# Kernel tuning notes

Measured on AMD Instinct MI355X. Metric: run time of the kernel, lower is better.

The kernel has to match this reference:

```python
import jax, jax.numpy as jnp
import numpy as np

N, E = 50000, 800000
C_IN, C_OUT, HID = 64, 64, 64


def setup_inputs() -> dict:
    key = jax.random.key(0)
    ks = jax.random.split(key, 12)
    def rn(k, shape, scale=0.05):
        return jax.random.normal(k, shape, dtype=jnp.float32) * scale
    return dict(
        x=jax.random.normal(ks[0], (N, C_IN), dtype=jnp.float32),
        pos=jax.random.normal(ks[1], (N, 3), dtype=jnp.float32),
        edge_index=jax.random.randint(ks[2], (2, E), 0, N),
        W_in=rn(ks[3], (C_IN, C_IN)), b_in=jnp.zeros((C_IN,), jnp.float32),
        W_out=rn(ks[4], (C_OUT, C_OUT)), b_out=jnp.zeros((C_OUT,), jnp.float32),
        W_lin=rn(ks[5], (C_OUT, C_IN)),   # PointTransformerConv.lin (value), bias=False
        W_src=rn(ks[6], (C_OUT, C_IN)),   # lin_src, bias=False
        W_dst=rn(ks[7], (C_OUT, C_IN)),   # lin_dst, bias=False
        pos_w1=rn(ks[8], (HID, 3)), pos_b1=jnp.zeros((HID,), jnp.float32),
        pos_w2=rn(ks[9], (C_OUT, HID)), pos_b2=jnp.zeros((C_OUT,), jnp.float32),
        att_w1=rn(ks[10], (HID, C_OUT)), att_b1=jnp.zeros((HID,), jnp.float32),
        att_w2=rn(ks[11], (C_OUT, HID)), att_b2=jnp.zeros((C_OUT,), jnp.float32),
    )


def _mlp2(y, w1, b1, w2, b2):
    # MLP([a, 64, b], batch_norm=False): Linear->ReLU->Linear->ReLU
    y = jax.nn.relu(y @ w1.T + b1)
    return jax.nn.relu(y @ w2.T + b2)


def reference(x, pos, edge_index, W_in, b_in, W_out, b_out, W_lin, W_src, W_dst,
              pos_w1, pos_b1, pos_w2, pos_b2, att_w1, att_b1, att_w2, att_b2):
    n = x.shape[0]
    h = jax.nn.relu(x @ W_in.T + b_in)            # lin_in + relu, (N, C_in)
    v = h @ W_lin.T                                # value projection (N, C_out)
    k_src = h @ W_src.T                            # alpha_j source part
    q_dst = h @ W_dst.T                            # alpha_i dest part
    # PointTransformerConv adds self-loops by default
    loop = jnp.arange(n)
    src = jnp.concatenate([edge_index[0], loop])   # (E+N,)
    dst = jnp.concatenate([edge_index[1], loop])
    # per-edge positional encoding: pos_nn(pos_i - pos_j)
    delta = _mlp2(pos[dst] - pos[src], pos_w1, pos_b1, pos_w2, pos_b2)
    # per-edge attention logits: attn_nn(alpha_i - alpha_j), (E+N, C_out)
    alpha = _mlp2(q_dst[dst] - k_src[src], att_w1, att_b1, att_w2, att_b2)
    # per-destination-node channelwise softmax (self-loops ensure no empty segment)
    amax = jax.ops.segment_max(alpha, dst, num_segments=n)
    ex = jnp.exp(alpha - amax[dst])
    denom = jax.ops.segment_sum(ex, dst, num_segments=n)
    w = ex / (denom[dst] + 1e-16)
    # message = alpha * (x_j + delta); aggregate = sum over neighbors
    out = jax.ops.segment_sum(w * (v[src] + delta), dst, num_segments=n)
    return jax.nn.relu(out @ W_out.T + b_out)
```

## Files before the change

### kernel.cpp

```cpp
#include <hip/hip_runtime.h>
#include <math.h>

#define NN 50000
#define EE 800000
#define ET (EE + NN)
#define C  64
#define NBLK 49
#define NCHUNK 831
#define ZBLK 463

typedef __attribute__((ext_vector_type(8))) _Float16 f16x8;
typedef __attribute__((ext_vector_type(4))) _Float16 f16x4;
typedef __attribute__((ext_vector_type(2))) _Float16 f16x2;
typedef __attribute__((ext_vector_type(4))) float f32x4;

__device__ __forceinline__ f16x2 pk2(float a, float b) {
  return __builtin_bit_cast(f16x2, __builtin_amdgcn_cvt_pkrtz(a, b));
}
__device__ __forceinline__ f16x4 pk4(float a, float b, float c, float d) {
  return __builtin_shufflevector(pk2(a, b), pk2(c, d), 0, 1, 2, 3);
}
__device__ __forceinline__ f16x8 pk8(const float* y) {
  const f16x4 lo = pk4(y[0], y[1], y[2], y[3]);
  const f16x4 hi = pk4(y[4], y[5], y[6], y[7]);
  return __builtin_shufflevector(lo, hi, 0, 1, 2, 3, 4, 5, 6, 7);
}

__device__ __forceinline__ f16x8 frag_ldh(const _Float16* base, int row,
                                          int kofs) {
  return *(const f16x8*)(base + row * 72 + kofs);
}
__device__ __forceinline__ void stage_w(_Float16* __restrict__ dst,
                                        const _Float16* __restrict__ src16,
                                        int tid) {
  const f16x8* src = (const f16x8*)(src16 + tid * 16);
  _Float16* d = dst + (tid >> 2) * 72 + (tid & 3) * 16;
  ((f16x8*)d)[0] = src[0];
  ((f16x8*)d)[1] = src[1];
}

__device__ __forceinline__ int swzb(int row, int colbyte) {
  return row * 128 + (colbyte ^ ((row & 7) << 4));
}
__device__ __forceinline__ f16x8 frag_lds(const _Float16* base, int row,
                                          int kofs) {
  return *(const f16x8*)((const char*)base + swzb(row, kofs * 2));
}
__device__ __forceinline__ void stage_ws(_Float16* __restrict__ dst,
                                         const _Float16* __restrict__ src16,
                                         int tid) {
  const f16x8* src = (const f16x8*)(src16 + tid * 16);
  const int row = tid >> 2;
  const int c0 = (tid & 3) * 32;
  *(f16x8*)((char*)dst + swzb(row, c0)) = src[0];
  *(f16x8*)((char*)dst + swzb(row, c0 + 16)) = src[1];
}

__device__ __forceinline__ int psl(int e, int o) {
  return (e + 2 * o + (o >> 5)) & 63;
}

__global__ __launch_bounds__(256) void prep_kernel(
    const float* __restrict__ W_in, const float* __restrict__ W_lin,
    const float* __restrict__ W_src, const float* __restrict__ W_dst,
    const float* __restrict__ att_w1, const float* __restrict__ att_w2,
    const float* __restrict__ pos_w2, const float* __restrict__ W_out,
    _Float16* __restrict__ w16, int* __restrict__ cnt2) {
  if (blockIdx.x < 8) {
    const float* Ws[8] = {W_in, W_lin, W_src, W_dst, att_w1, att_w2, pos_w2,
                          W_out};
    const float* src = Ws[blockIdx.x];
    _Float16* dst = w16 + blockIdx.x * 4096;
    const float sc = (blockIdx.x == 5) ? 1.44269504088896340736f : 1.0f;
#pragma unroll
    for (int i = threadIdx.x * 4; i < 4096; i += 1024) {
      const float4 w = *(const float4*)(src + i);
      *(f16x4*)(dst + i) = pk4(w.x * sc, w.y * sc, w.z * sc, w.w * sc);
    }
  }
  int4* cz = (int4*)cnt2;
#pragma unroll 1
  for (int i = blockIdx.x * 256 + threadIdx.x; i < 2 * NN; i += 64 * 256)
    cz[i] = make_int4(0, 0, 0, 0);
}

__global__ __launch_bounds__(256) void scan_partial(const int* __restrict__ cnt2,
                                                    int* __restrict__ bsum,
                                                    float* __restrict__ zeroreg) {
  const int t = threadIdx.x;
  if (blockIdx.x >= NBLK) {
    const int zb = blockIdx.x - NBLK;
    float4* dst = (float4*)zeroreg;
    const int total4 = 2 * NN * 64 / 4;
    const float4 z = make_float4(0.f, 0.f, 0.f, 0.f);
#pragma unroll 1
    for (int i = zb * 256 + t; i < total4; i += ZBLK * 256) dst[i] = z;
    return;
  }
  __shared__ int ws[4];
  const int base = blockIdx.x * 1024 + t * 4;
  int s = 0;
  if (base + 3 < NN) {
#pragma unroll
    for (int sh = 0; sh < 8; ++sh) {
      const int4 v = *(const int4*)(cnt2 + sh * NN + base);
      s += v.x + v.y + v.z + v.w;
    }
  } else {
#pragma unroll
    for (int i = 0; i < 4; ++i)
      if (base + i < NN)
#pragma unroll
        for (int sh = 0; sh < 8; ++sh) s += cnt2[sh * NN + base + i];
  }
#pragma unroll
  for (int off = 32; off; off >>= 1) s += __shfl_down(s, off, 64);
  if ((t & 63) == 0) ws[t >> 6] = s;
  __syncthreads();
  if (t == 0) bsum[blockIdx.x] = ws[0] + ws[1] + ws[2] + ws[3];
}

__global__ __launch_bounds__(256) void scan_final(const int* __restrict__ cnt2,
                                                  const int* __restrict__ bsum,
                                                  int* __restrict__ curs2) {
  __shared__ int tsum[256];
  __shared__ int sblk[64];
  const int t = threadIdx.x;
  if (t < 64) {
    const int mine = (t < NBLK) ? bsum[t] : 0;
    int v = mine;
#pragma unroll
    for (int off = 1; off < 64; off <<= 1) {
      const int u = __shfl_up(v, off, 64);
      if (t >= off) v += u;
    }
    sblk[t] = v - mine;
  }
  const int base = blockIdx.x * 1024 + t * 4;
  int c2[8][4];
  int v[4] = {0, 0, 0, 0};
  if (base + 3 < NN) {
#pragma unroll
    for (int sh = 0; sh < 8; ++sh) {
      const int4 x = *(const int4*)(cnt2 + sh * NN + base);
      c2[sh][0] = x.x; c2[sh][1] = x.y; c2[sh][2] = x.z; c2[sh][3] = x.w;
      v[0] += x.x; v[1] += x.y; v[2] += x.z; v[3] += x.w;
    }
  } else {
#pragma unroll
    for (int sh = 0; sh < 8; ++sh)
#pragma unroll
      for (int i = 0; i < 4; ++i) {
        const int c = (base + i < NN) ? cnt2[sh * NN + base + i] : 0;
        c2[sh][i] = c;
        v[i] += c;
      }
  }
  const int s = v[0] + v[1] + v[2] + v[3];
  tsum[t] = s;
  __syncthreads();
  for (int off = 1; off < 256; off <<= 1) {
    const int u = (t >= off) ? tsum[t - off] : 0;
    __syncthreads();
    tsum[t] += u;
    __syncthreads();
  }
  int ex = sblk[blockIdx.x] + tsum[t] - s;
  int offs[8][4];
#pragma unroll
  for (int i = 0; i < 4; ++i) {
    int run = ex;
#pragma unroll
    for (int sh = 0; sh < 8; ++sh) {
      offs[sh][i] = run;
      run += c2[sh][i];
    }
    ex += v[i];
  }
  if (base + 3 < NN) {
#pragma unroll
    for (int sh = 0; sh < 8; ++sh)
      *(int4*)(curs2 + sh * NN + base) =
          make_int4(offs[sh][0], offs[sh][1], offs[sh][2], offs[sh][3]);
  } else {
#pragma unroll
    for (int sh = 0; sh < 8; ++sh)
#pragma unroll
      for (int i = 0; i < 4; ++i)
        if (base + i < NN) curs2[sh * NN + base + i] = offs[sh][i];
  }
}

__global__ __launch_bounds__(256) void scatter_kernel(const int* __restrict__ ei,
                                                      int* __restrict__ curs2,
                                                      int2* __restrict__ srt) {
  const int chunk = blockIdx.x;
  int* cs = curs2 + (chunk & 7) * NN;
  const int e0 = chunk * 1024 + threadIdx.x * 4;
  if (e0 >= ET) return;
  int s[4], d[4];
  if (e0 + 3 < EE) {
    const int4 sv = *(const int4*)(ei + e0);
    const int4 dv = *(const int4*)(ei + EE + e0);
    s[0] = sv.x; s[1] = sv.y; s[2] = sv.z; s[3] = sv.w;
    d[0] = dv.x; d[1] = dv.y; d[2] = dv.z; d[3] = dv.w;
  } else {
#pragma unroll
    for (int i = 0; i < 4; ++i) {
      const int e = e0 + i;
      if (e < EE) {
        s[i] = ei[e];
        d[i] = ei[EE + e];
      } else if (e < ET) {
        s[i] = d[i] = e - EE;
      } else {
        s[i] = d[i] = -1;
      }
    }
  }
#pragma unroll
  for (int i = 0; i < 4; ++i) {
    if (d[i] >= 0) {
      const int p = atomicAdd(&cs[d[i]], 1);
      srt[p] = make_int2(s[i], d[i]);
    }
  }
}

__global__ __launch_bounds__(256, 3) void node_proj(
    const float* __restrict__ x, const float* __restrict__ b_in,
    const _Float16* __restrict__ w16, const int* __restrict__ ei,
    int* __restrict__ cnt2, _Float16* __restrict__ vh,
    _Float16* __restrict__ kh, _Float16* __restrict__ qh) {
  __shared__ __align__(16) _Float16 wlds[4 * 4608];
  __shared__ __align__(16) _Float16 hlds[4608];
  __shared__ float biasv[64];

  const int tid = threadIdx.x;
  const int nb = blockIdx.x * 64;
  const int l15 = tid & 15;
  const int quad = (tid >> 4) & 3;
  const int wband = tid >> 6;
  const int nloc = wband * 16 + l15;
  const int gn = nb + nloc;

#pragma unroll 1
  for (int chunk = blockIdx.x; chunk < NCHUNK; chunk += gridDim.x) {
    int* cs = cnt2 + (chunk & 7) * NN;
    const int e0 = chunk * 1024 + tid * 4;
    if (e0 < ET) {
      int d[4];
      if (e0 + 3 < EE) {
        const int4 dv = *(const int4*)(ei + EE + e0);
        d[0] = dv.x; d[1] = dv.y; d[2] = dv.z; d[3] = dv.w;
      } else {
#pragma unroll
        for (int i = 0; i < 4; ++i) {
          const int e = e0 + i;
          d[i] = (e < EE) ? ei[EE + e] : ((e < ET) ? e - EE : -1);
        }
      }
#pragma unroll
      for (int i = 0; i < 4; ++i)
        if (d[i] >= 0) atomicAdd(&cs[d[i]], 1);
    }
  }

#pragma unroll
  for (int w = 0; w < 4; ++w) stage_w(wlds + w * 4608, w16 + w * 4096, tid);
  if (tid < 64) biasv[tid] = b_in[tid];

  f16x8 bfrag[2];
#pragma unroll
  for (int ks = 0; ks < 2; ++ks) {
    float y[8] = {0.f, 0.f, 0.f, 0.f, 0.f, 0.f, 0.f, 0.f};
    if (gn < NN) {
      const float4 a = *(const float4*)(x + (size_t)gn * 64 + ks * 32 + quad * 8);
      const float4 b = *(const float4*)(x + (size_t)gn * 64 + ks * 32 + quad * 8 + 4);
      y[0] = a.x; y[1] = a.y; y[2] = a.z; y[3] = a.w;
      y[4] = b.x; y[5] = b.y; y[6] = b.z; y[7] = b.w;
    }
    bfrag[ks] = pk8(y);
  }
  __syncthreads();

#pragma unroll
  for (int t = 0; t < 4; ++t) {
    f32x4 acc = {0.f, 0.f, 0.f, 0.f};
#pragma unroll
    for (int ks = 0; ks < 2; ++ks) {
      const f16x8 af = frag_ldh(wlds, t * 16 + l15, ks * 32 + quad * 8);
      acc = __builtin_amdgcn_mfma_f32_16x16x32_f16(af, bfrag[ks], acc, 0, 0, 0);
    }
    const int hb = t * 16 + quad * 4;
    *(f16x4*)(hlds + nloc * 72 + hb) =
        pk4(fmaxf(acc[0] + biasv[hb + 0], 0.f), fmaxf(acc[1] + biasv[hb + 1], 0.f),
            fmaxf(acc[2] + biasv[hb + 2], 0.f), fmaxf(acc[3] + biasv[hb + 3], 0.f));
  }
  __syncthreads();

  f16x8 hfrag[2];
#pragma unroll
  for (int ks = 0; ks < 2; ++ks)
    hfrag[ks] = frag_ldh(hlds, nloc, ks * 32 + quad * 8);

  _Float16* outs[3] = {vh, kh, qh};
#pragma unroll
  for (int p = 0; p < 3; ++p) {
    const _Float16* W = wlds + (p + 1) * 4608;
#pragma unroll
    for (int t = 0; t < 4; ++t) {
      f32x4 acc = {0.f, 0.f, 0.f, 0.f};
#pragma unroll
      for (int ks = 0; ks < 2; ++ks) {
        const f16x8 af = frag_ldh(W, t * 16 + l15, ks * 32 + quad * 8);
        acc = __builtin_amdgcn_mfma_f32_16x16x32_f16(af, hfrag[ks], acc, 0, 0, 0);
      }
      if (gn < NN) {
        *(f16x4*)(outs[p] + (size_t)gn * 64 + t * 16 + quad * 4) =
            pk4(acc[0], acc[1], acc[2], acc[3]);
      }
    }
  }
}

__global__ __launch_bounds__(256, 6) void edge_pass(
    const int2* __restrict__ srt, const float* __restrict__ pos,
    const _Float16* __restrict__ vh, const _Float16* __restrict__ kh,
    const _Float16* __restrict__ qh, const _Float16* __restrict__ w16,
    const float* __restrict__ att_b1, const float* __restrict__ att_b2,
    const float* __restrict__ pos_w1, const float* __restrict__ pos_b1,
    const float* __restrict__ pos_b2, float* __restrict__ num,
    float* __restrict__ den) {
  __shared__ __align__(16) _Float16 smem[12288];
  __shared__ __align__(16) float posw1T[3 * 64];
  __shared__ float b1s[64], b2s[64], pb1s[64], pb2s[64];
  __shared__ int dsts[64];

  _Float16* W1 = smem;
  _Float16* W2 = smem + 4096;
  _Float16* HP = smem + 8192;
  f16x2* pairb = (f16x2*)smem;

  const int tid = threadIdx.x;
  const int eb = blockIdx.x * 64;
  const int l15 = tid & 15;
  const int quad = (tid >> 4) & 3;
  const int wband = tid >> 6;
  const int eloc = wband * 16 + l15;

  int s_mine, d_mine;
  f16x8 bfrag[2];
  float dp0, dp1, dp2;
  {
    const int e = eb + eloc;
    int2 sd = make_int2(0, 0);
    int valid_d = -1;
    if (e < ET) {
      sd = srt[e];
      valid_d = sd.y;
    }
    s_mine = sd.x;
    d_mine = sd.y;
    if (quad == 0) dsts[eloc] = valid_d;
#pragma unroll
    for (int ks = 0; ks < 2; ++ks) {
      const f16x8 qv =
          *(const f16x8*)(qh + (size_t)d_mine * 64 + ks * 32 + quad * 8);
      const f16x8 kv =
          *(const f16x8*)(kh + (size_t)s_mine * 64 + ks * 32 + quad * 8);
      bfrag[ks] = qv - kv;
    }
    dp0 = pos[(size_t)d_mine * 3 + 0] - pos[(size_t)s_mine * 3 + 0];
    dp1 = pos[(size_t)d_mine * 3 + 1] - pos[(size_t)s_mine * 3 + 1];
    dp2 = pos[(size_t)d_mine * 3 + 2] - pos[(size_t)s_mine * 3 + 2];
  }

  stage_ws(W1, w16 + 4 * 4096, tid);
  stage_ws(W2, w16 + 5 * 4096, tid);
  if (tid < 64) {
    b1s[tid] = att_b1[tid];
    b2s[tid] = att_b2[tid] * 1.44269504088896340736f;
    pb1s[tid] = pos_b1[tid];
    pb2s[tid] = pos_b2[tid];
    posw1T[0 * 64 + tid] = pos_w1[tid * 3 + 0];
    posw1T[1 * 64 + tid] = pos_w1[tid * 3 + 1];
    posw1T[2 * 64 + tid] = pos_w1[tid * 3 + 2];
  }
  __syncthreads();

#pragma unroll
  for (int t = 0; t < 4; ++t) {
    f32x4 acc = {0.f, 0.f, 0.f, 0.f};
#pragma unroll
    for (int ks = 0; ks < 2; ++ks) {
      const f16x8 af = frag_lds(W1, t * 16 + l15, ks * 32 + quad * 8);
      acc = __builtin_amdgcn_mfma_f32_16x16x32_f16(af, bfrag[ks], acc, 0, 0, 0);
    }
    const int hb = t * 16 + quad * 4;
    *(f16x4*)((char*)HP + swzb(eloc, hb * 2)) =
        pk4(fmaxf(acc[0] + b1s[hb + 0], 0.f), fmaxf(acc[1] + b1s[hb + 1], 0.f),
            fmaxf(acc[2] + b1s[hb + 2], 0.f), fmaxf(acc[3] + b1s[hb + 3], 0.f));
  }

  f16x8 hpfrag[2];
#pragma unroll
  for (int ks = 0; ks < 2; ++ks) {
    float hv[8];
#pragma unroll
    for (int j = 0; j < 8; ++j) {
      const int i = ks * 32 + quad * 8 + j;
      float h = pb1s[i];
      h = fmaf(dp0, posw1T[i], h);
      h = fmaf(dp1, posw1T[64 + i], h);
      h = fmaf(dp2, posw1T[128 + i], h);
      hv[j] = fmaxf(h, 0.f);
    }
    hpfrag[ks] = pk8(hv);
  }

  float ex[16];
  {
    f16x8 hfrag[2];
#pragma unroll
    for (int ks = 0; ks < 2; ++ks)
      hfrag[ks] = frag_lds(HP, eloc, ks * 32 + quad * 8);
#pragma unroll
    for (int t = 0; t < 4; ++t) {
      f32x4 acc = {0.f, 0.f, 0.f, 0.f};
#pragma unroll
      for (int ks = 0; ks < 2; ++ks) {
        const f16x8 af = frag_lds(W2, t * 16 + l15, ks * 32 + quad * 8);
        acc = __builtin_amdgcn_mfma_f32_16x16x32_f16(af, hfrag[ks], acc, 0, 0, 0);
      }
      const int ob = t * 16 + quad * 4;
#pragma unroll
      for (int r = 0; r < 4; ++r)
        ex[t * 4 + r] = __builtin_exp2f(fmaxf(acc[r] + b2s[ob + r], 0.f));
    }
  }
  float vr[16];
#pragma unroll
  for (int t = 0; t < 4; ++t) {
    const f16x4 v4 = *(const f16x4*)(vh + (size_t)s_mine * 64 + t * 16 + quad * 4);
    vr[t * 4 + 0] = (float)v4[0];
    vr[t * 4 + 1] = (float)v4[1];
    vr[t * 4 + 2] = (float)v4[2];
    vr[t * 4 + 3] = (float)v4[3];
  }
  __syncthreads();

  stage_ws(HP, w16 + 6 * 4096, tid);
  __syncthreads();

  float del[16];
#pragma unroll
  for (int t = 0; t < 4; ++t) {
    f32x4 acc = {0.f, 0.f, 0.f, 0.f};
#pragma unroll
    for (int ks = 0; ks < 2; ++ks) {
      const f16x8 af = frag_lds(HP, t * 16 + l15, ks * 32 + quad * 8);
      acc = __builtin_amdgcn_mfma_f32_16x16x32_f16(af, hpfrag[ks], acc, 0, 0, 0);
    }
    const int ob = t * 16 + quad * 4;
#pragma unroll
    for (int r = 0; r < 4; ++r)
      del[t * 4 + r] = fmaxf(acc[r] + pb2s[ob + r], 0.f);
  }

#pragma unroll
  for (int t = 0; t < 4; ++t) {
#pragma unroll
    for (int r = 0; r < 4; ++r) {
      const int o = t * 16 + quad * 4 + r;
      const float e_ = ex[t * 4 + r];
      pairb[o * 64 + psl(eloc, o)] =
          pk2(e_ * (vr[t * 4 + r] + del[t * 4 + r]), e_);
    }
  }
  __syncthreads();

  {
    const int c = tid & 63;
    const int r = tid >> 6;
    float am = 0.f, ae = 0.f;
    int cur = -1;
#pragma unroll 1
    for (int t2 = 0; t2 < 16; ++t2) {
      const int el = r * 16 + t2;
      const int d = dsts[el];
      if (d != cur) {
        if (cur >= 0) {
          unsafeAtomicAdd(num + (size_t)cur * 64 + c, am);
          unsafeAtomicAdd(den + (size_t)cur * 64 + c, ae);
        }
        cur = d;
        am = 0.f;
        ae = 0.f;
      }
      if (d >= 0) {
        const f16x2 pe = pairb[c * 64 + psl(el, c)];
        am += (float)pe[0];
        ae += (float)pe[1];
      }
    }
    if (cur >= 0) {
      unsafeAtomicAdd(num + (size_t)cur * 64 + c, am);
      unsafeAtomicAdd(den + (size_t)cur * 64 + c, ae);
    }
  }
}

__global__ __launch_bounds__(256, 4) void out_proj(
    const float* __restrict__ num, const float* __restrict__ den,
    const _Float16* __restrict__ w16, const float* __restrict__ b_out,
    float* __restrict__ out) {
  __shared__ __align__(16) _Float16 wlds[4608];
  __shared__ float biasv[64];

  const int tid = threadIdx.x;
  const int nb = blockIdx.x * 64;
  const int l15 = tid & 15;
  const int quad = (tid >> 4) & 3;
  const int wband = tid >> 6;
  const int gn = nb + wband * 16 + l15;

  stage_w(wlds, w16 + 7 * 4096, tid);
  if (tid < 64) biasv[tid] = b_out[tid];

  f16x8 bfrag[2];
#pragma unroll
  for (int ks = 0; ks < 2; ++ks) {
    float y[8] = {0.f, 0.f, 0.f, 0.f, 0.f, 0.f, 0.f, 0.f};
    if (gn < NN) {
      const size_t base = (size_t)gn * 64 + ks * 32 + quad * 8;
      const float4 n0 = *(const float4*)(num + base);
      const float4 n1 = *(const float4*)(num + base + 4);
      const float4 d0 = *(const float4*)(den + base);
      const float4 d1 = *(const float4*)(den + base + 4);
      y[0] = n0.x / (d0.x + 1e-16f); y[1] = n0.y / (d0.y + 1e-16f);
      y[2] = n0.z / (d0.z + 1e-16f); y[3] = n0.w / (d0.w + 1e-16f);
      y[4] = n1.x / (d1.x + 1e-16f); y[5] = n1.y / (d1.y + 1e-16f);
      y[6] = n1.z / (d1.z + 1e-16f); y[7] = n1.w / (d1.w + 1e-16f);
    }
    bfrag[ks] = pk8(y);
  }
  __syncthreads();

#pragma unroll
  for (int t = 0; t < 4; ++t) {
    f32x4 acc = {0.f, 0.f, 0.f, 0.f};
#pragma unroll
    for (int ks = 0; ks < 2; ++ks) {
      const f16x8 af = frag_ldh(wlds, t * 16 + l15, ks * 32 + quad * 8);
      acc = __builtin_amdgcn_mfma_f32_16x16x32_f16(af, bfrag[ks], acc, 0, 0, 0);
    }
    if (gn < NN) {
      const int ob = t * 16 + quad * 4;
      float4 r;
      r.x = fmaxf(acc[0] + biasv[ob + 0], 0.f);
      r.y = fmaxf(acc[1] + biasv[ob + 1], 0.f);
      r.z = fmaxf(acc[2] + biasv[ob + 2], 0.f);
      r.w = fmaxf(acc[3] + biasv[ob + 3], 0.f);
      *(float4*)(out + (size_t)gn * 64 + ob) = r;
    }
  }
}

extern "C" void kernel_launch(void* const* d_in, const int* in_sizes, int n_in,
                              void* d_out, int out_size, void* d_ws,
                              size_t ws_size, hipStream_t stream) {
  const float* x      = (const float*)d_in[0];
  const float* pos    = (const float*)d_in[1];
  const int*   ei     = (const int*)d_in[2];
  const float* W_in   = (const float*)d_in[3];
  const float* b_in   = (const float*)d_in[4];
  const float* W_out  = (const float*)d_in[5];
  const float* b_out  = (const float*)d_in[6];
  const float* W_lin  = (const float*)d_in[7];
  const float* W_src  = (const float*)d_in[8];
  const float* W_dst  = (const float*)d_in[9];
  const float* pos_w1 = (const float*)d_in[10];
  const float* pos_b1 = (const float*)d_in[11];
  const float* pos_w2 = (const float*)d_in[12];
  const float* pos_b2 = (const float*)d_in[13];
  const float* att_w1 = (const float*)d_in[14];
  const float* att_b1 = (const float*)d_in[15];
  const float* att_w2 = (const float*)d_in[16];
  const float* att_b2 = (const float*)d_in[17];

  float* ws = (float*)d_ws;
  const size_t NC = (size_t)NN * C;
  float* num = ws;
  float* den = ws + NC;
  _Float16* vh = (_Float16*)(ws + 2 * NC);
  _Float16* kh = vh + NC;
  _Float16* qh = kh + NC;
  _Float16* w16 = qh + NC;
  int* ib     = (int*)(w16 + 8 * 4096);
  int* cnt2   = ib;
  int* curs2  = ib + 8 * NN;
  int* bsum   = ib + 16 * NN;
  int2* srt   = (int2*)(((uintptr_t)(bsum + NBLK) + 15) & ~(uintptr_t)15);

  const dim3 blk(256);
  prep_kernel<<<dim3(64), blk, 0, stream>>>(W_in, W_lin, W_src, W_dst, att_w1,
                                            att_w2, pos_w2, W_out, w16, cnt2);
  node_proj<<<dim3((NN + 63) / 64), blk, 0, stream>>>(x, b_in, w16, ei, cnt2,
                                                      vh, kh, qh);
  scan_partial<<<dim3(NBLK + ZBLK), blk, 0, stream>>>(cnt2, bsum, num);
  scan_final<<<dim3(NBLK), blk, 0, stream>>>(cnt2, bsum, curs2);
  scatter_kernel<<<dim3(NCHUNK), blk, 0, stream>>>(ei, curs2, srt);
  edge_pass<<<dim3((ET + 63) / 64), blk, 0, stream>>>(
      srt, pos, vh, kh, qh, w16, att_b1, att_b2, pos_w1, pos_b1, pos_b2, num,
      den);
  out_proj<<<dim3((NN + 63) / 64), blk, 0, stream>>>(num, den, w16, b_out,
                                                     (float*)d_out);
}
```

Measured before the change: 291.5 us.

## Double edge_pass block to 128 edges with 512 threads and reuse shared memory

The edge pass now processes 128 edges per block with 512 threads instead of 64 edges with 256 threads. Staging of the attention and positional-MLP weights is therefore spread over twice as many edges. The positional weight matrix now reuses the first attention weight buffer, and an extra barrier was added because the enlarged pair buffer overlaps it. Launch bounds change to 512 threads with a higher occupancy hint, which may raise register pressure and cause spills. The extra barrier and larger per-block shared memory footprint could also reduce overlap between blocks.

```diff
diff --git a/kernel.cpp b/kernel.cpp
--- a/kernel.cpp
+++ b/kernel.cpp
@@ -8,6 +8,8 @@
 #define NBLK 49
 #define NCHUNK 831
 #define ZBLK 463
+#define EB 128
+#define NEBLK ((ET + EB - 1) / EB)
 
 typedef __attribute__((ext_vector_type(8))) _Float16 f16x8;
 typedef __attribute__((ext_vector_type(4))) _Float16 f16x4;
@@ -46,18 +48,15 @@
                                           int kofs) {
   return *(const f16x8*)((const char*)base + swzb(row, kofs * 2));
 }
-__device__ __forceinline__ void stage_ws(_Float16* __restrict__ dst,
-                                         const _Float16* __restrict__ src16,
-                                         int tid) {
-  const f16x8* src = (const f16x8*)(src16 + tid * 16);
-  const int row = tid >> 2;
-  const int c0 = (tid & 3) * 32;
-  *(f16x8*)((char*)dst + swzb(row, c0)) = src[0];
-  *(f16x8*)((char*)dst + swzb(row, c0 + 16)) = src[1];
+__device__ __forceinline__ void stage_ws512(_Float16* __restrict__ dst,
+                                            const _Float16* __restrict__ src16,
+                                            int tid) {
+  const f16x8 v = *(const f16x8*)(src16 + tid * 8);
+  *(f16x8*)((char*)dst + swzb(tid >> 3, (tid & 7) * 16)) = v;
 }
 
 __device__ __forceinline__ int psl(int e, int o) {
-  return (e + 2 * o + (o >> 5)) & 63;
+  return (e + 2 * o + (o >> 5)) & 127;
 }
 
 __global__ __launch_bounds__(256) void prep_kernel(
@@ -324,7 +323,7 @@
   }
 }
 
-__global__ __launch_bounds__(256, 6) void edge_pass(
+__global__ __launch_bounds__(512, 8) void edge_pass(
     const int2* __restrict__ srt, const float* __restrict__ pos,
     const _Float16* __restrict__ vh, const _Float16* __restrict__ kh,
     const _Float16* __restrict__ qh, const _Float16* __restrict__ w16,
@@ -332,10 +331,10 @@
     const float* __restrict__ pos_w1, const float* __restrict__ pos_b1,
     const float* __restrict__ pos_b2, float* __restrict__ num,
     float* __restrict__ den) {
-  __shared__ __align__(16) _Float16 smem[12288];
+  __shared__ __align__(16) _Float16 smem[16384];
   __shared__ __align__(16) float posw1T[3 * 64];
   __shared__ float b1s[64], b2s[64], pb1s[64], pb2s[64];
-  __shared__ int dsts[64];
+  __shared__ int dsts[EB];
 
   _Float16* W1 = smem;
   _Float16* W2 = smem + 4096;
@@ -343,7 +342,7 @@
   f16x2* pairb = (f16x2*)smem;
 
   const int tid = threadIdx.x;
-  const int eb = blockIdx.x * 64;
+  const int eb = blockIdx.x * EB;
   const int l15 = tid & 15;
   const int quad = (tid >> 4) & 3;
   const int wband = tid >> 6;
@@ -376,8 +375,8 @@
     dp2 = pos[(size_t)d_mine * 3 + 2] - pos[(size_t)s_mine * 3 + 2];
   }
 
-  stage_ws(W1, w16 + 4 * 4096, tid);
-  stage_ws(W2, w16 + 5 * 4096, tid);
+  stage_ws512(W1, w16 + 4 * 4096, tid);
+  stage_ws512(W2, w16 + 5 * 4096, tid);
   if (tid < 64) {
     b1s[tid] = att_b1[tid];
     b2s[tid] = att_b2[tid] * 1.44269504088896340736f;
@@ -450,7 +449,7 @@
   }
   __syncthreads();
 
-  stage_ws(HP, w16 + 6 * 4096, tid);
+  stage_ws512(W1, w16 + 6 * 4096, tid);
   __syncthreads();
 
   float del[16];
@@ -459,7 +458,7 @@
     f32x4 acc = {0.f, 0.f, 0.f, 0.f};
 #pragma unroll
     for (int ks = 0; ks < 2; ++ks) {
-      const f16x8 af = frag_lds(HP, t * 16 + l15, ks * 32 + quad * 8);
+      const f16x8 af = frag_lds(W1, t * 16 + l15, ks * 32 + quad * 8);
       acc = __builtin_amdgcn_mfma_f32_16x16x32_f16(af, hpfrag[ks], acc, 0, 0, 0);
     }
     const int ob = t * 16 + quad * 4;
@@ -467,6 +466,7 @@
     for (int r = 0; r < 4; ++r)
       del[t * 4 + r] = fmaxf(acc[r] + pb2s[ob + r], 0.f);
   }
+  __syncthreads();
 
 #pragma unroll
   for (int t = 0; t < 4; ++t) {
@@ -474,7 +474,7 @@
     for (int r = 0; r < 4; ++r) {
       const int o = t * 16 + quad * 4 + r;
       const float e_ = ex[t * 4 + r];
-      pairb[o * 64 + psl(eloc, o)] =
+      pairb[o * EB + psl(eloc, o)] =
           pk2(e_ * (vr[t * 4 + r] + del[t * 4 + r]), e_);
     }
   }
@@ -499,7 +499,7 @@
         ae = 0.f;
       }
       if (d >= 0) {
-        const f16x2 pe = pairb[c * 64 + psl(el, c)];
+        const f16x2 pe = pairb[c * EB + psl(el, c)];
         am += (float)pe[0];
         ae += (float)pe[1];
       }
@@ -611,7 +611,7 @@
   scan_partial<<<dim3(NBLK + ZBLK), blk, 0, stream>>>(cnt2, bsum, num);
   scan_final<<<dim3(NBLK), blk, 0, stream>>>(cnt2, bsum, curs2);
   scatter_kernel<<<dim3(NCHUNK), blk, 0, stream>>>(ei, curs2, srt);
-  edge_pass<<<dim3((ET + 63) / 64), blk, 0, stream>>>(
+  edge_pass<<<dim3(NEBLK), dim3(512), 0, stream>>>(
       srt, pos, vh, kh, qh, w16, att_b1, att_b2, pos_w1, pos_b1, pos_b2, num,
       den);
   out_proj<<<dim3((NN + 63) / 64), blk, 0, stream>>>(num, den, w16, b_out,
```

Measured after the change: 305.1 us. +4.7%, slower.

## Swap MFMA operands so edge results land per-channel and scatter from registers

Applied to the files above, without the earlier changes.

The second attention MLP layer and the positional MLP layer now pass activations as the A operand and weights as B. Each lane therefore holds four consecutive edges for one channel, and the segmented reduction and atomics run straight from registers. This removes the shared-memory pair buffer transpose and one barrier, and the value rows are gathered per channel up front. The cost is shorter run merging: only four edges per lane instead of sixteen per thread, which may mean more atomic operations, and the per-element 2-byte value gathers are less coalesced.

```diff
diff --git a/kernel.cpp b/kernel.cpp
--- a/kernel.cpp
+++ b/kernel.cpp
@@ -54,10 +54,6 @@
   const int c0 = (tid & 3) * 32;
   *(f16x8*)((char*)dst + swzb(row, c0)) = src[0];
   *(f16x8*)((char*)dst + swzb(row, c0 + 16)) = src[1];
-}
-
-__device__ __forceinline__ int psl(int e, int o) {
-  return (e + 2 * o + (o >> 5)) & 63;
 }
 
 __global__ __launch_bounds__(256) void prep_kernel(
@@ -336,11 +332,11 @@
   __shared__ __align__(16) float posw1T[3 * 64];
   __shared__ float b1s[64], b2s[64], pb1s[64], pb2s[64];
   __shared__ int dsts[64];
+  __shared__ int srcs[64];
 
   _Float16* W1 = smem;
   _Float16* W2 = smem + 4096;
   _Float16* HP = smem + 8192;
-  f16x2* pairb = (f16x2*)smem;
 
   const int tid = threadIdx.x;
   const int eb = blockIdx.x * 64;
@@ -362,7 +358,10 @@
     }
     s_mine = sd.x;
     d_mine = sd.y;
-    if (quad == 0) dsts[eloc] = valid_d;
+    if (quad == 0) {
+      dsts[eloc] = valid_d;
+      srcs[eloc] = sd.x;
+    }
 #pragma unroll
     for (int ks = 0; ks < 2; ++ks) {
       const f16x8 qv =
@@ -389,6 +388,27 @@
   }
   __syncthreads();
 
+  int d4[4], s4[4];
+#pragma unroll
+  for (int r = 0; r < 4; ++r) {
+    d4[r] = dsts[wband * 16 + quad * 4 + r];
+    s4[r] = srcs[wband * 16 + quad * 4 + r];
+  }
+  _Float16 vvh[16];
+#pragma unroll
+  for (int r = 0; r < 4; ++r) {
+    const int sr = (d4[r] >= 0) ? s4[r] : 0;
+    const _Float16* vp = vh + (size_t)sr * 64 + l15;
+#pragma unroll
+    for (int tc = 0; tc < 4; ++tc) vvh[tc * 4 + r] = vp[tc * 16];
+  }
+  float b2v[4], pb2v[4];
+#pragma unroll
+  for (int tc = 0; tc < 4; ++tc) {
+    b2v[tc] = b2s[tc * 16 + l15];
+    pb2v[tc] = pb2s[tc * 16 + l15];
+  }
+
 #pragma unroll
   for (int t = 0; t < 4; ++t) {
     f32x4 acc = {0.f, 0.f, 0.f, 0.f};
@@ -419,94 +439,67 @@
     hpfrag[ks] = pk8(hv);
   }
 
-  float ex[16];
+  float exq[16];
   {
     f16x8 hfrag[2];
 #pragma unroll
     for (int ks = 0; ks < 2; ++ks)
       hfrag[ks] = frag_lds(HP, eloc, ks * 32 + quad * 8);
 #pragma unroll
-    for (int t = 0; t < 4; ++t) {
+    for (int tc = 0; tc < 4; ++tc) {
       f32x4 acc = {0.f, 0.f, 0.f, 0.f};
 #pragma unroll
       for (int ks = 0; ks < 2; ++ks) {
-        const f16x8 af = frag_lds(W2, t * 16 + l15, ks * 32 + quad * 8);
-        acc = __builtin_amdgcn_mfma_f32_16x16x32_f16(af, hfrag[ks], acc, 0, 0, 0);
-      }
-      const int ob = t * 16 + quad * 4;
+        const f16x8 bw = frag_lds(W2, tc * 16 + l15, ks * 32 + quad * 8);
+        acc = __builtin_amdgcn_mfma_f32_16x16x32_f16(hfrag[ks], bw, acc, 0, 0, 0);
+      }
 #pragma unroll
       for (int r = 0; r < 4; ++r)
-        ex[t * 4 + r] = __builtin_exp2f(fmaxf(acc[r] + b2s[ob + r], 0.f));
-    }
-  }
-  float vr[16];
-#pragma unroll
-  for (int t = 0; t < 4; ++t) {
-    const f16x4 v4 = *(const f16x4*)(vh + (size_t)s_mine * 64 + t * 16 + quad * 4);
-    vr[t * 4 + 0] = (float)v4[0];
-    vr[t * 4 + 1] = (float)v4[1];
-    vr[t * 4 + 2] = (float)v4[2];
-    vr[t * 4 + 3] = (float)v4[3];
-  }
-  __syncthreads();
-
-  stage_ws(HP, w16 + 6 * 4096, tid);
-  __syncthreads();
-
-  float del[16];
-#pragma unroll
-  for (int t = 0; t < 4; ++t) {
+        exq[tc * 4 + r] = __builtin_exp2f(fmaxf(acc[r] + b2v[tc], 0.f));
+    }
+  }
+  __syncthreads();
+
+  stage_ws(W1, w16 + 6 * 4096, tid);
+  __syncthreads();
+
+#pragma unroll
+  for (int tc = 0; tc < 4; ++tc) {
     f32x4 acc = {0.f, 0.f, 0.f, 0.f};
 #pragma unroll
     for (int ks = 0; ks < 2; ++ks) {
-      const f16x8 af = frag_lds(HP, t * 16 + l15, ks * 32 + quad * 8);
-      acc = __builtin_amdgcn_mfma_f32_16x16x32_f16(af, hpfrag[ks], acc, 0, 0, 0);
-    }
-    const int ob = t * 16 + quad * 4;
-#pragma unroll
-    for (int r = 0; r < 4; ++r)
-      del[t * 4 + r] = fmaxf(acc[r] + pb2s[ob + r], 0.f);
-  }
-
-#pragma unroll
-  for (int t = 0; t < 4; ++t) {
+      const f16x8 bw = frag_lds(W1, tc * 16 + l15, ks * 32 + quad * 8);
+      acc = __builtin_amdgcn_mfma_f32_16x16x32_f16(hpfrag[ks], bw, acc, 0, 0, 0);
+    }
+    const int ch = tc * 16 + l15;
+    float m4[4], e4[4];
 #pragma unroll
     for (int r = 0; r < 4; ++r) {
-      const int o = t * 16 + quad * 4 + r;
-      const float e_ = ex[t * 4 + r];
-      pairb[o * 64 + psl(eloc, o)] =
-          pk2(e_ * (vr[t * 4 + r] + del[t * 4 + r]), e_);
-    }
-  }
-  __syncthreads();
-
-  {
-    const int c = tid & 63;
-    const int r = tid >> 6;
+      const float del = fmaxf(acc[r] + pb2v[tc], 0.f);
+      e4[r] = exq[tc * 4 + r];
+      m4[r] = e4[r] * ((float)vvh[tc * 4 + r] + del);
+    }
     float am = 0.f, ae = 0.f;
-    int cur = -1;
-#pragma unroll 1
-    for (int t2 = 0; t2 < 16; ++t2) {
-      const int el = r * 16 + t2;
-      const int d = dsts[el];
-      if (d != cur) {
+    int cur = d4[0];
+#pragma unroll
+    for (int r = 0; r < 4; ++r) {
+      if (d4[r] != cur) {
         if (cur >= 0) {
-          unsafeAtomicAdd(num + (size_t)cur * 64 + c, am);
-          unsafeAtomicAdd(den + (size_t)cur * 64 + c, ae);
+          unsafeAtomicAdd(num + (size_t)cur * 64 + ch, am);
+          unsafeAtomicAdd(den + (size_t)cur * 64 + ch, ae);
         }
-        cur = d;
         am = 0.f;
         ae = 0.f;
-      }
-      if (d >= 0) {
-        const f16x2 pe = pairb[c * 64 + psl(el, c)];
-        am += (float)pe[0];
-        ae += (float)pe[1];
+        cur = d4[r];
+      }
+      if (d4[r] >= 0) {
+        am += m4[r];
+        ae += e4[r];
       }
     }
     if (cur >= 0) {
-      unsafeAtomicAdd(num + (size_t)cur * 64 + c, am);
-      unsafeAtomicAdd(den + (size_t)cur * 64 + c, ae);
+      unsafeAtomicAdd(num + (size_t)cur * 64 + ch, am);
+      unsafeAtomicAdd(den + (size_t)cur * 64 + ch, ae);
     }
   }
 }
```

After: 476.0 us. 63.3% more time.
